# Optimization experiments

Measured on AMD Instinct MI355X. Metric: run time of the kernel, lower is better.

The kernel has to match this reference:

```python
import jax, jax.numpy as jnp
import numpy as np

LMAX = 4  # number of l blocks (lmax+1 in the original)
# segment ids mapping the L2 = sum(2l+1) = 16 spherical components to their l block
SEG = np.repeat(np.arange(LMAX), 2 * np.arange(LMAX) + 1)  # [16]
SEG_ONEHOT = np.eye(LMAX, dtype=np.float32)[SEG]  # [16, LMAX]


def setup_inputs() -> dict:
    key = jax.random.key(0)
    ks = jax.random.split(key, 10)
    b, m, f, k, L2 = 16, 64, 128, 64, 16
    def rnd(kk, shape, scale):
        return jax.random.normal(kk, shape, dtype=jnp.float32) * scale
    return {
        'x': rnd(ks[0], (b, m, f, L2), 1.0),
        'y': rnd(ks[1], (b, m, f, L2), 1.0),
        'wx0': rnd(ks[2], (k, f, f, LMAX), 1.0 / np.sqrt(f * f * LMAX)),
        'wy0': rnd(ks[3], (k, f, f, LMAX), 1.0 / np.sqrt(f * f * LMAX)),
        'wx_mlp': rnd(ks[4], (2, k, k), 1.0 / np.sqrt(k)),
        'bx_mlp': rnd(ks[5], (2, k, k), 0.02),
        'wy_mlp': rnd(ks[6], (2, k, k), 1.0 / np.sqrt(k)),
        'by_mlp': rnd(ks[7], (2, k, k), 0.02),
        'wxf': rnd(ks[8], (LMAX, f, k), 1.0 / np.sqrt(k)),
        'wyf': rnd(ks[9], (LMAX, f, k), 1.0 / np.sqrt(k)),
    }


def reference(x, y, wx0, wy0, wx_mlp, bx_mlp, wy_mlp, by_mlp, wxf, wyf):
    act = jax.nn.silu
    S = jnp.asarray(SEG_ONEHOT)  # [L2, lmax]
    # outer product of y and x features, segment-summed over each l block:
    # mix[b,m,fy,fx,l] = sum_c y[b,m,fy,c] * x[b,m,fx,c] * S[c,l]
    mix = jnp.einsum('bmfc,bmgc,cl->bmfgl', y, x, S)  # [b,m,f,f,lmax]
    mx = jnp.einsum('bmfgl,kfgl->bmk', mix, wx0)
    my = jnp.einsum('bmfgl,kfgl->bmk', mix, wy0)
    for i in range(wx_mlp.shape[0]):  # the n_mlp-1 used MLP stages
        mx = act(jnp.einsum('bmk,kl->bml', mx, wx_mlp[i]) + bx_mlp[i])
        my = act(jnp.einsum('bmk,kl->bml', my, wy_mlp[i]) + by_mlp[i])
    mx = act(jnp.einsum('bmk,lfk->bmfl', mx, wxf))  # [b,m,f,lmax]
    my = act(jnp.einsum('bmk,lfk->bmfl', my, wyf))
    # broadcast each l gate over its 2l+1 components (repeat == gather by SEG)
    seg = jnp.asarray(SEG)
    res = mx[..., seg] * x + my[..., seg] * y  # [b,m,f,L2]
    return res
```

## Files before the change

kernel.cpp:

```cpp
#include <hip/hip_runtime.h>
#include <stdint.h>


#define AS1 __attribute__((address_space(1)))
#define AS3 __attribute__((address_space(3)))

typedef __bf16 bf16x8 __attribute__((ext_vector_type(8)));
typedef float f32x4 __attribute__((ext_vector_type(4)));

__device__ __forceinline__ uint16_t f2b(float f) {
  uint32_t u = __float_as_uint(f);
  u += 0x7fffu + ((u >> 16) & 1u);
  return (uint16_t)(u >> 16);
}

#if __has_builtin(__builtin_amdgcn_fdot2_f32_bf16)
typedef __bf16 bf16x2 __attribute__((ext_vector_type(2)));
__device__ __forceinline__ float dot2b(uint32_t a, uint32_t b, float c) {
  union { uint32_t u; bf16x2 v; } ua, ub;
  ua.u = a; ub.u = b;
  return __builtin_amdgcn_fdot2_f32_bf16(ua.v, ub.v, c, false);
}
#else
__device__ __forceinline__ float dot2b(uint32_t a, uint32_t b, float c) {
  float a0 = __uint_as_float(a << 16), a1 = __uint_as_float(a & 0xffff0000u);
  float b0 = __uint_as_float(b << 16), b1 = __uint_as_float(b & 0xffff0000u);
  return c + a0 * b0 + a1 * b1;
}
#endif

__global__ __launch_bounds__(256) void convert_all(
    const float* __restrict__ wx0, const float* __restrict__ wy0,
    const float* __restrict__ x, const float* __restrict__ y,
    const float* __restrict__ wxf, const float* __restrict__ wyf,
    uint16_t* __restrict__ Wb2, uint16_t* __restrict__ xb,
    uint16_t* __restrict__ yb, float* __restrict__ wfT) {
  int bid = blockIdx.x, tid = threadIdx.x;
  if (bid < 4096) {
    int c = bid * 256 + tid;
    int fb = c >> 16;
    int rem = c & 65535;
    int fy = rem >> 9;
    int rem2 = rem & 511;
    int n = rem2 >> 2, pos = rem2 & 3;
    int slot = pos ^ ((n >> 1) & 3);
    int k = n & 63;
    const float* src = (n < 64 ? wx0 : wy0) +
        ((size_t)(k * 128 + fy) * 512 + fb * 32 + slot * 8);
    float4 v0 = *(const float4*)src;
    float4 v1 = *(const float4*)(src + 4);
    uint32_t o0 = (uint32_t)f2b(v0.x) | ((uint32_t)f2b(v0.y) << 16);
    uint32_t o1 = (uint32_t)f2b(v0.z) | ((uint32_t)f2b(v0.w) << 16);
    uint32_t o2 = (uint32_t)f2b(v1.x) | ((uint32_t)f2b(v1.y) << 16);
    uint32_t o3 = (uint32_t)f2b(v1.z) | ((uint32_t)f2b(v1.w) << 16);
    *(uint4*)(Wb2 + (size_t)c * 8) = make_uint4(o0, o1, o2, o3);
    return;
  }
  if (bid >= 6144) {
    int base = (bid - 6144) * 2048 + tid * 8;
#pragma unroll
    for (int ii = 0; ii < 8; ++ii) {
      int idx = base + ii;
      int side = idx >> 15, rem = idx & 32767;
      int k = rem >> 9, l = (rem >> 7) & 3, f = rem & 127;
      const float* src = side ? wyf : wxf;
      wfT[idx] = src[((size_t)l * 128 + f) * 64 + k];
    }
    return;
  }
  size_t i = ((size_t)(bid - 4096) * 256 + tid) * 8;
  const float* s; uint16_t* d;
  if (i < 2097152) { s = x + i;             d = xb + i; }
  else             { s = y + (i - 2097152); d = yb + (i - 2097152); }
  float4 v0 = *(const float4*)s;
  float4 v1 = *(const float4*)(s + 4);
  uint32_t o0 = (uint32_t)f2b(v0.x) | ((uint32_t)f2b(v0.y) << 16);
  uint32_t o1 = (uint32_t)f2b(v0.z) | ((uint32_t)f2b(v0.w) << 16);
  uint32_t o2 = (uint32_t)f2b(v1.x) | ((uint32_t)f2b(v1.y) << 16);
  uint32_t o3 = (uint32_t)f2b(v1.z) | ((uint32_t)f2b(v1.w) << 16);
  *(uint4*)d = make_uint4(o0, o1, o2, o3);
}

__device__ __forceinline__ void gload_lds16(const void* g, void* l) {
  __builtin_amdgcn_global_load_lds((const AS1 uint32_t*)g, (AS3 uint32_t*)l, 16, 0, 0);
}

#define PIPE_BAR(N) \
  asm volatile("s_waitcnt vmcnt(" #N ") lgkmcnt(0)\n\ts_barrier" ::: "memory")

__global__ __launch_bounds__(512, 4) void fused_gemm(
    const uint16_t* __restrict__ xb, const uint16_t* __restrict__ yb,
    const uint16_t* __restrict__ Wb2, float* __restrict__ Cpart) {
  __shared__ __align__(16) uint16_t sA[2][128 * 32];
  __shared__ __align__(16) uint16_t sB[3][128 * 32];
  __shared__ __align__(16) uint16_t yS[3][2048];

  int tid = threadIdx.x;
  int w = tid >> 6, lane = tid & 63;
  int g_id = blockIdx.x;
  int fb = g_id >> 2, fyg = g_id & 3;
  int FB = fb * 8;
  int fy0 = fyg * 32;
  int m0 = blockIdx.y * 128;
  int r = lane & 15, q = lane >> 4;
  int wm = w >> 2, wn = w & 3;
  int m_loc = tid & 127, quarter = tid >> 7;

  uint32_t xr[16];
  {
    const uint16_t* xp0 = xb + (size_t)(m0 + m_loc) * 2048 + (FB + quarter * 2) * 16;
#pragma unroll
    for (int j = 0; j < 4; ++j) {
      uint4 v = *(const uint4*)(xp0 + j * 8);
      xr[j * 4 + 0] = v.x; xr[j * 4 + 1] = v.y;
      xr[j * 4 + 2] = v.z; xr[j * 4 + 3] = v.w;
    }
  }

  f32x4 zero = {0.f, 0.f, 0.f, 0.f};
  f32x4 acc[4][2];
#pragma unroll
  for (int i = 0; i < 4; ++i)
#pragma unroll
    for (int j = 0; j < 2; ++j) acc[i][j] = zero;

  auto issueB = [&](uint16_t* dstB, int t) {
    if (w < 4) {
      size_t base = (size_t)(fb * 128 + fy0 + t) * 4096;
#pragma unroll
      for (int jj = 0; jj < 2; ++jj) {
        int blk = w * 2 + jj;
        gload_lds16(Wb2 + base + blk * 512 + lane * 8, dstB + blk * 512);
      }
    }
  };
  int ychunk = (w >> 1) & 1, ymbase = (w & 1) * 64;
  const uint16_t* ysrc_base = yb + (size_t)(m0 + ymbase + lane) * 2048 + ychunk * 8;
  int ydst_off = ychunk * 1024 + ymbase * 8;
  auto issueY = [&](uint16_t* dstY, int t) {
    if (w >= 4) gload_lds16(ysrc_base + (size_t)(fy0 + t) * 16, dstY + ydst_off);
  };

  auto computeG = [&](const uint16_t* srcY, float* gg) {
    uint4 ya = *(const uint4*)(srcY + m_loc * 8);
    uint4 yc = *(const uint4*)(srcY + 1024 + m_loc * 8);
    uint32_t yp[8] = {ya.x, ya.y, ya.z, ya.w, yc.x, yc.y, yc.z, yc.w};
    uint32_t yl0 = yp[0] & 0xffffu, yh0 = yp[0] & 0xffff0000u;
    uint32_t yl4 = yp[4] & 0xffffu, yh4 = yp[4] & 0xffff0000u;
#pragma unroll
    for (int fxp = 0; fxp < 2; ++fxp) {
      const uint32_t* xp = xr + fxp * 8;
      gg[fxp * 4 + 0] = dot2b(xp[0], yl0, 0.f);
      gg[fxp * 4 + 1] = dot2b(xp[1], yp[1], dot2b(xp[0], yh0, 0.f));
      gg[fxp * 4 + 2] = dot2b(xp[4], yl4,
                         dot2b(xp[3], yp[3], dot2b(xp[2], yp[2], 0.f)));
      gg[fxp * 4 + 3] = dot2b(xp[7], yp[7], dot2b(xp[6], yp[6],
                         dot2b(xp[5], yp[5], dot2b(xp[4], yh4, 0.f))));
    }
  };
  auto writeA = [&](uint16_t* dstA, const float* gg) {
    uint32_t o[4];
#pragma unroll
    for (int p = 0; p < 4; ++p)
      o[p] = (__float_as_uint(gg[2 * p]) >> 16) |
             (__float_as_uint(gg[2 * p + 1]) & 0xffff0000u);
    int pos = quarter ^ ((m_loc >> 1) & 3);
    *(uint4*)(dstA + m_loc * 32 + pos * 8) = make_uint4(o[0], o[1], o[2], o[3]);
  };

  float gg[8];
  issueY(yS[0], 0);
  __syncthreads();
  computeG(yS[0], gg);
  writeA(sA[0], gg);
  issueB(sB[0], 0);
  issueY(yS[1], 1);
  issueB(sB[1], 1);
  issueY(yS[2], 2);
  if (w < 4) PIPE_BAR(2); else PIPE_BAR(1);

  uint16_t *pAc = sA[0], *pAn = sA[1];
  uint16_t *pBread = sB[0], *pBmid = sB[1], *pBissue = sB[2];
  uint16_t *pYcomp = yS[1], *pYmid = yS[2], *pYissue = yS[0];

  for (int t = 0; t < 32; ++t) {
    if (t <= 29) issueB(pBissue, t + 2);
    if (t <= 28) issueY(pYissue, t + 3);

    bf16x8 a[4], b[2];
#pragma unroll
    for (int i = 0; i < 4; ++i) {
      int row = wm * 64 + i * 16 + r;
      int pos = q ^ ((row >> 1) & 3);
      a[i] = *(const bf16x8*)&pAc[row * 32 + pos * 8];
    }
#pragma unroll
    for (int j = 0; j < 2; ++j) {
      int row = wn * 32 + j * 16 + r;
      int pos = q ^ ((row >> 1) & 3);
      b[j] = *(const bf16x8*)&pBread[row * 32 + pos * 8];
    }

    if (t < 31) {
      computeG(pYcomp, gg);
      writeA(pAn, gg);
    }

    __builtin_amdgcn_s_setprio(1);
#pragma unroll
    for (int i = 0; i < 4; ++i)
#pragma unroll
      for (int j = 0; j < 2; ++j)
        acc[i][j] = __builtin_amdgcn_mfma_f32_16x16x32_bf16(a[i], b[j], acc[i][j], 0, 0, 0);
    __builtin_amdgcn_s_setprio(0);

    if (t <= 28)      { if (w < 4) PIPE_BAR(2); else PIPE_BAR(1); }
    else if (t == 29) { if (w < 4) PIPE_BAR(2); else PIPE_BAR(0); }
    else if (t == 30) PIPE_BAR(0);

    uint16_t* tp;
    tp = pAc; pAc = pAn; pAn = tp;
    tp = pBread; pBread = pBmid; pBmid = pBissue; pBissue = tp;
    tp = pYcomp; pYcomp = pYmid; pYmid = pYissue; pYissue = tp;
  }

  float* cbase = Cpart + (size_t)g_id * 131072;
#pragma unroll
  for (int i = 0; i < 4; ++i)
#pragma unroll
    for (int j = 0; j < 2; ++j)
#pragma unroll
      for (int reg = 0; reg < 4; ++reg) {
        int mm = m0 + wm * 64 + i * 16 + q * 4 + reg;
        int nn = wn * 32 + j * 16 + r;
        cbase[(size_t)mm * 128 + nn] = acc[i][j][reg];
      }
}

__global__ __launch_bounds__(256) void finish_kernel(
    const float* __restrict__ x, const float* __restrict__ y,
    const float* __restrict__ wx_mlp, const float* __restrict__ bx_mlp,
    const float* __restrict__ wy_mlp, const float* __restrict__ by_mlp,
    const float* __restrict__ wfT,
    const float* __restrict__ Cpart, float* __restrict__ out) {
  const int seg[16] = {0,1,1,1,2,2,2,2,2,3,3,3,3,3,3,3};
  __shared__ float sred[256];
  __shared__ float sm[128];
  __shared__ float sg[2][128][4];
  int t = threadIdx.x;
  int bm = blockIdx.x;
  int mi = bm & 63;

  {
    int col = t & 127, hh = t >> 7;
    const float* cp = Cpart + (size_t)(hh * 32) * 131072 + (size_t)bm * 128 + col;
    float s = 0.f;
#pragma unroll 8
    for (int sp = 0; sp < 32; ++sp)
      s += cp[(size_t)sp * 131072];
    sred[t] = s;
  }
  __syncthreads();
  if (t < 128) sm[t] = sred[t] + sred[t + 128];
  __syncthreads();

  for (int st = 0; st < 2; ++st) {
    float v = 0.f;
    if (t < 128) {
      int side = t >> 6, j = t & 63;
      const float* wmlp = side ? wy_mlp : wx_mlp;
      const float* bmlp = side ? by_mlp : bx_mlp;
      const float* mv = sm + side * 64;
#pragma unroll 8
      for (int k = 0; k < 64; ++k)
        v += mv[k] * wmlp[(st * 64 + k) * 64 + j];
      v += bmlp[(st * 64 + mi) * 64 + j];
      v = v / (1.f + __expf(-v));
    }
    __syncthreads();
    if (t < 128) sm[t] = v;
    __syncthreads();
  }

  {
    int side = t >> 7, f = t & 127;
    const float* base = wfT + side * 32768;
    const float* mv = sm + side * 64;
    float gg[4] = {0.f, 0.f, 0.f, 0.f};
#pragma unroll 8
    for (int k = 0; k < 64; ++k) {
      float m2 = mv[k];
#pragma unroll
      for (int l = 0; l < 4; ++l)
        gg[l] += m2 * base[(k * 4 + l) * 128 + f];
    }
#pragma unroll
    for (int l = 0; l < 4; ++l)
      sg[side][f][l] = gg[l] / (1.f + __expf(-gg[l]));
  }
  __syncthreads();

  {
    int f = t >> 1, half = t & 1;
    size_t base = ((size_t)bm * 128 + f) * 16 + half * 8;
    float4 xa = *(const float4*)(x + base), xb4 = *(const float4*)(x + base + 4);
    float4 ya = *(const float4*)(y + base), yb4 = *(const float4*)(y + base + 4);
    float xv[8] = {xa.x, xa.y, xa.z, xa.w, xb4.x, xb4.y, xb4.z, xb4.w};
    float yv[8] = {ya.x, ya.y, ya.z, ya.w, yb4.x, yb4.y, yb4.z, yb4.w};
    float o[8];
#pragma unroll
    for (int ii = 0; ii < 8; ++ii) {
      int c = half * 8 + ii;
      o[ii] = sg[0][f][seg[c]] * xv[ii] + sg[1][f][seg[c]] * yv[ii];
    }
    *(float4*)(out + base)     = make_float4(o[0], o[1], o[2], o[3]);
    *(float4*)(out + base + 4) = make_float4(o[4], o[5], o[6], o[7]);
  }
}

extern "C" void kernel_launch(void* const* d_in, const int* in_sizes, int n_in,
                              void* d_out, int out_size, void* d_ws, size_t ws_size,
                              hipStream_t stream) {
  const float* x      = (const float*)d_in[0];
  const float* y      = (const float*)d_in[1];
  const float* wx0    = (const float*)d_in[2];
  const float* wy0    = (const float*)d_in[3];
  const float* wx_mlp = (const float*)d_in[4];
  const float* bx_mlp = (const float*)d_in[5];
  const float* wy_mlp = (const float*)d_in[6];
  const float* by_mlp = (const float*)d_in[7];
  const float* wxf    = (const float*)d_in[8];
  const float* wyf    = (const float*)d_in[9];
  float* out = (float*)d_out;

  uint16_t* Wb2   = (uint16_t*)d_ws;
  uint16_t* xb    = (uint16_t*)((char*)d_ws + (size_t)16777216);
  uint16_t* yb    = (uint16_t*)((char*)d_ws + (size_t)20971520);
  float*    Cpart = (float*)((char*)d_ws + (size_t)25165824);
  float*    wfT   = (float*)((char*)d_ws + (size_t)58720256);

  convert_all<<<6176, 256, 0, stream>>>(wx0, wy0, x, y, wxf, wyf, Wb2, xb, yb, wfT);
  fused_gemm<<<dim3(64, 8), 512, 0, stream>>>(xb, yb, Wb2, Cpart);
  finish_kernel<<<1024, 256, 0, stream>>>(x, y, wx_mlp, bx_mlp, wy_mlp, by_mlp,
                                          wfT, Cpart, out);
}
```

Baseline: 166.1 us.

## Build GEMM A operand in registers, drop LDS staging, halve M tile

The fused GEMM now computes the segment-summed outer-product A fragments directly in each wave's registers, in the MFMA operand layout, and feeds them straight to MFMA. This removes the sA LDS buffer and its write/read round trip. Blocks shrink to 256 threads with 64-row M tiles, giving twice as many blocks, and the y and W loads are re-pipelined with two stages in flight. The weight conversion now reads the source contiguously and scatters its writes, so global reads are coalesced. In exchange each wave recomputes the A values it needs and holds more x data in registers.

```diff
diff --git a/kernel.cpp b/kernel.cpp
--- a/kernel.cpp
+++ b/kernel.cpp
@@ -37,23 +37,25 @@
     uint16_t* __restrict__ yb, float* __restrict__ wfT) {
   int bid = blockIdx.x, tid = threadIdx.x;
   if (bid < 4096) {
-    int c = bid * 256 + tid;
-    int fb = c >> 16;
-    int rem = c & 65535;
-    int fy = rem >> 9;
-    int rem2 = rem & 511;
-    int n = rem2 >> 2, pos = rem2 & 3;
-    int slot = pos ^ ((n >> 1) & 3);
-    int k = n & 63;
-    const float* src = (n < 64 ? wx0 : wy0) +
-        ((size_t)(k * 128 + fy) * 512 + fb * 32 + slot * 8);
+    size_t idx = ((size_t)bid * 256 + tid) * 8;
+    int side = idx >= 4194304 ? 1 : 0;
+    size_t rem = side ? idx - 4194304 : idx;
+    const float* src = (side ? wy0 : wx0) + rem;
     float4 v0 = *(const float4*)src;
     float4 v1 = *(const float4*)(src + 4);
+    int fx0 = (int)((rem >> 2) & 127);
+    int fy  = (int)((rem >> 9) & 127);
+    int k   = (int)(rem >> 16);
+    int n = side * 64 + k;
+    int fb = fx0 >> 3;
+    int slot = (fx0 >> 1) & 3;
+    int pos = slot ^ ((n >> 1) & 3);
     uint32_t o0 = (uint32_t)f2b(v0.x) | ((uint32_t)f2b(v0.y) << 16);
     uint32_t o1 = (uint32_t)f2b(v0.z) | ((uint32_t)f2b(v0.w) << 16);
     uint32_t o2 = (uint32_t)f2b(v1.x) | ((uint32_t)f2b(v1.y) << 16);
     uint32_t o3 = (uint32_t)f2b(v1.z) | ((uint32_t)f2b(v1.w) << 16);
-    *(uint4*)(Wb2 + (size_t)c * 8) = make_uint4(o0, o1, o2, o3);
+    size_t chunk = (((size_t)(fb * 128 + fy)) * 128 + n) * 4 + pos;
+    *(uint4*)(Wb2 + chunk * 8) = make_uint4(o0, o1, o2, o3);
     return;
   }
   if (bid >= 6144) {
@@ -88,12 +90,11 @@
 #define PIPE_BAR(N) \
   asm volatile("s_waitcnt vmcnt(" #N ") lgkmcnt(0)\n\ts_barrier" ::: "memory")
 
-__global__ __launch_bounds__(512, 4) void fused_gemm(
+__global__ __launch_bounds__(256, 4) void fused_gemm(
     const uint16_t* __restrict__ xb, const uint16_t* __restrict__ yb,
     const uint16_t* __restrict__ Wb2, float* __restrict__ Cpart) {
-  __shared__ __align__(16) uint16_t sA[2][128 * 32];
   __shared__ __align__(16) uint16_t sB[3][128 * 32];
-  __shared__ __align__(16) uint16_t yS[3][2048];
+  __shared__ __align__(16) uint16_t yS[3][1024];
 
   int tid = threadIdx.x;
   int w = tid >> 6, lane = tid & 63;
@@ -101,138 +102,114 @@
   int fb = g_id >> 2, fyg = g_id & 3;
   int FB = fb * 8;
   int fy0 = fyg * 32;
-  int m0 = blockIdx.y * 128;
+  int m0 = blockIdx.y * 64;
   int r = lane & 15, q = lane >> 4;
-  int wm = w >> 2, wn = w & 3;
-  int m_loc = tid & 127, quarter = tid >> 7;
-
-  uint32_t xr[16];
-  {
-    const uint16_t* xp0 = xb + (size_t)(m0 + m_loc) * 2048 + (FB + quarter * 2) * 16;
+  int wm = w >> 1, wn = w & 1;
+
+  uint32_t xreg[2][16];
+#pragma unroll
+  for (int i = 0; i < 2; ++i) {
+    const uint16_t* xp0 =
+        xb + (size_t)(m0 + wm * 32 + i * 16 + r) * 2048 + (FB + 2 * q) * 16;
+#pragma unroll
+    for (int j2 = 0; j2 < 4; ++j2) {
+      uint4 v = *(const uint4*)(xp0 + j2 * 8);
+      xreg[i][j2 * 4 + 0] = v.x; xreg[i][j2 * 4 + 1] = v.y;
+      xreg[i][j2 * 4 + 2] = v.z; xreg[i][j2 * 4 + 3] = v.w;
+    }
+  }
+
+  f32x4 zero = {0.f, 0.f, 0.f, 0.f};
+  f32x4 acc[2][4];
+#pragma unroll
+  for (int i = 0; i < 2; ++i)
+#pragma unroll
+    for (int j = 0; j < 4; ++j) acc[i][j] = zero;
+
+  int fbfy = fb * 128 + fy0;
+  auto issueB = [&](uint16_t* dstB, int t) {
+    size_t base = (size_t)(fbfy + t) * 4096;
+    gload_lds16(Wb2 + base + (size_t)(w * 2) * 512 + lane * 8,
+                dstB + (w * 2) * 512);
+    gload_lds16(Wb2 + base + (size_t)(w * 2 + 1) * 512 + lane * 8,
+                dstB + (w * 2 + 1) * 512);
+  };
+  const uint16_t* ysrc = yb + (size_t)(m0 + lane) * 2048 + w * 8;
+  auto issueY = [&](uint16_t* dstY, int t) {
+    if (w < 2) gload_lds16(ysrc + (size_t)(fy0 + t) * 16, dstY + w * 512);
+  };
+
+  issueB(sB[0], 0); issueY(yS[0], 0);
+  issueB(sB[1], 1); issueY(yS[1], 1);
+  if (w < 2) PIPE_BAR(3); else PIPE_BAR(2);
+
+  uint16_t *pB0 = sB[0], *pB1 = sB[1], *pB2 = sB[2];
+  uint16_t *pY0 = yS[0], *pY1 = yS[1], *pY2 = yS[2];
+
+  for (int t = 0; t < 32; ++t) {
+    if (t <= 29) { issueB(pB2, t + 2); issueY(pY2, t + 2); }
+
+    bf16x8 b[4];
 #pragma unroll
     for (int j = 0; j < 4; ++j) {
-      uint4 v = *(const uint4*)(xp0 + j * 8);
-      xr[j * 4 + 0] = v.x; xr[j * 4 + 1] = v.y;
-      xr[j * 4 + 2] = v.z; xr[j * 4 + 3] = v.w;
-    }
-  }
-
-  f32x4 zero = {0.f, 0.f, 0.f, 0.f};
-  f32x4 acc[4][2];
-#pragma unroll
-  for (int i = 0; i < 4; ++i)
-#pragma unroll
-    for (int j = 0; j < 2; ++j) acc[i][j] = zero;
-
-  auto issueB = [&](uint16_t* dstB, int t) {
-    if (w < 4) {
-      size_t base = (size_t)(fb * 128 + fy0 + t) * 4096;
-#pragma unroll
-      for (int jj = 0; jj < 2; ++jj) {
-        int blk = w * 2 + jj;
-        gload_lds16(Wb2 + base + blk * 512 + lane * 8, dstB + blk * 512);
+      int row = wn * 64 + j * 16 + r;
+      int pos = q ^ ((row >> 1) & 3);
+      b[j] = *(const bf16x8*)&pB0[row * 32 + pos * 8];
+    }
+    uint32_t yw[2][8];
+#pragma unroll
+    for (int i = 0; i < 2; ++i) {
+      int row = wm * 32 + i * 16 + r;
+      uint4 a0 = *(const uint4*)&pY0[row * 8];
+      uint4 a1 = *(const uint4*)&pY0[512 + row * 8];
+      yw[i][0] = a0.x; yw[i][1] = a0.y; yw[i][2] = a0.z; yw[i][3] = a0.w;
+      yw[i][4] = a1.x; yw[i][5] = a1.y; yw[i][6] = a1.z; yw[i][7] = a1.w;
+    }
+
+#pragma unroll
+    for (int i = 0; i < 2; ++i) {
+      uint32_t yl0 = yw[i][0] & 0xffffu, yh0 = yw[i][0] & 0xffff0000u;
+      uint32_t yl4 = yw[i][4] & 0xffffu, yh4 = yw[i][4] & 0xffff0000u;
+      union { uint32_t u[4]; bf16x8 v; } af;
+#pragma unroll
+      for (int fxp = 0; fxp < 2; ++fxp) {
+        const uint32_t* xp = &xreg[i][fxp * 8];
+        float g0 = dot2b(xp[0], yl0, 0.f);
+        float g1 = dot2b(xp[1], yw[i][1], dot2b(xp[0], yh0, 0.f));
+        float g2 = dot2b(xp[4], yl4,
+                    dot2b(xp[3], yw[i][3], dot2b(xp[2], yw[i][2], 0.f)));
+        float g3 = dot2b(xp[7], yw[i][7], dot2b(xp[6], yw[i][6],
+                    dot2b(xp[5], yw[i][5], dot2b(xp[4], yh4, 0.f))));
+        af.u[fxp * 2 + 0] = (__float_as_uint(g0) >> 16) |
+                            (__float_as_uint(g1) & 0xffff0000u);
+        af.u[fxp * 2 + 1] = (__float_as_uint(g2) >> 16) |
+                            (__float_as_uint(g3) & 0xffff0000u);
       }
-    }
-  };
-  int ychunk = (w >> 1) & 1, ymbase = (w & 1) * 64;
-  const uint16_t* ysrc_base = yb + (size_t)(m0 + ymbase + lane) * 2048 + ychunk * 8;
-  int ydst_off = ychunk * 1024 + ymbase * 8;
-  auto issueY = [&](uint16_t* dstY, int t) {
-    if (w >= 4) gload_lds16(ysrc_base + (size_t)(fy0 + t) * 16, dstY + ydst_off);
-  };
-
-  auto computeG = [&](const uint16_t* srcY, float* gg) {
-    uint4 ya = *(const uint4*)(srcY + m_loc * 8);
-    uint4 yc = *(const uint4*)(srcY + 1024 + m_loc * 8);
-    uint32_t yp[8] = {ya.x, ya.y, ya.z, ya.w, yc.x, yc.y, yc.z, yc.w};
-    uint32_t yl0 = yp[0] & 0xffffu, yh0 = yp[0] & 0xffff0000u;
-    uint32_t yl4 = yp[4] & 0xffffu, yh4 = yp[4] & 0xffff0000u;
-#pragma unroll
-    for (int fxp = 0; fxp < 2; ++fxp) {
-      const uint32_t* xp = xr + fxp * 8;
-      gg[fxp * 4 + 0] = dot2b(xp[0], yl0, 0.f);
-      gg[fxp * 4 + 1] = dot2b(xp[1], yp[1], dot2b(xp[0], yh0, 0.f));
-      gg[fxp * 4 + 2] = dot2b(xp[4], yl4,
-                         dot2b(xp[3], yp[3], dot2b(xp[2], yp[2], 0.f)));
-      gg[fxp * 4 + 3] = dot2b(xp[7], yp[7], dot2b(xp[6], yp[6],
-                         dot2b(xp[5], yp[5], dot2b(xp[4], yh4, 0.f))));
-    }
-  };
-  auto writeA = [&](uint16_t* dstA, const float* gg) {
-    uint32_t o[4];
-#pragma unroll
-    for (int p = 0; p < 4; ++p)
-      o[p] = (__float_as_uint(gg[2 * p]) >> 16) |
-             (__float_as_uint(gg[2 * p + 1]) & 0xffff0000u);
-    int pos = quarter ^ ((m_loc >> 1) & 3);
-    *(uint4*)(dstA + m_loc * 32 + pos * 8) = make_uint4(o[0], o[1], o[2], o[3]);
-  };
-
-  float gg[8];
-  issueY(yS[0], 0);
-  __syncthreads();
-  computeG(yS[0], gg);
-  writeA(sA[0], gg);
-  issueB(sB[0], 0);
-  issueY(yS[1], 1);
-  issueB(sB[1], 1);
-  issueY(yS[2], 2);
-  if (w < 4) PIPE_BAR(2); else PIPE_BAR(1);
-
-  uint16_t *pAc = sA[0], *pAn = sA[1];
-  uint16_t *pBread = sB[0], *pBmid = sB[1], *pBissue = sB[2];
-  uint16_t *pYcomp = yS[1], *pYmid = yS[2], *pYissue = yS[0];
-
-  for (int t = 0; t < 32; ++t) {
-    if (t <= 29) issueB(pBissue, t + 2);
-    if (t <= 28) issueY(pYissue, t + 3);
-
-    bf16x8 a[4], b[2];
-#pragma unroll
-    for (int i = 0; i < 4; ++i) {
-      int row = wm * 64 + i * 16 + r;
-      int pos = q ^ ((row >> 1) & 3);
-      a[i] = *(const bf16x8*)&pAc[row * 32 + pos * 8];
-    }
-#pragma unroll
-    for (int j = 0; j < 2; ++j) {
-      int row = wn * 32 + j * 16 + r;
-      int pos = q ^ ((row >> 1) & 3);
-      b[j] = *(const bf16x8*)&pBread[row * 32 + pos * 8];
-    }
-
-    if (t < 31) {
-      computeG(pYcomp, gg);
-      writeA(pAn, gg);
-    }
-
-    __builtin_amdgcn_s_setprio(1);
-#pragma unroll
-    for (int i = 0; i < 4; ++i)
-#pragma unroll
-      for (int j = 0; j < 2; ++j)
-        acc[i][j] = __builtin_amdgcn_mfma_f32_16x16x32_bf16(a[i], b[j], acc[i][j], 0, 0, 0);
-    __builtin_amdgcn_s_setprio(0);
-
-    if (t <= 28)      { if (w < 4) PIPE_BAR(2); else PIPE_BAR(1); }
-    else if (t == 29) { if (w < 4) PIPE_BAR(2); else PIPE_BAR(0); }
+      __builtin_amdgcn_s_setprio(1);
+#pragma unroll
+      for (int j = 0; j < 4; ++j)
+        acc[i][j] = __builtin_amdgcn_mfma_f32_16x16x32_bf16(af.v, b[j],
+                                                            acc[i][j], 0, 0, 0);
+      __builtin_amdgcn_s_setprio(0);
+    }
+
+    if (t <= 29)      { if (w < 2) PIPE_BAR(3); else PIPE_BAR(2); }
     else if (t == 30) PIPE_BAR(0);
 
     uint16_t* tp;
-    tp = pAc; pAc = pAn; pAn = tp;
-    tp = pBread; pBread = pBmid; pBmid = pBissue; pBissue = tp;
-    tp = pYcomp; pYcomp = pYmid; pYmid = pYissue; pYissue = tp;
+    tp = pB0; pB0 = pB1; pB1 = pB2; pB2 = tp;
+    tp = pY0; pY0 = pY1; pY1 = pY2; pY2 = tp;
   }
 
   float* cbase = Cpart + (size_t)g_id * 131072;
 #pragma unroll
-  for (int i = 0; i < 4; ++i)
-#pragma unroll
-    for (int j = 0; j < 2; ++j)
+  for (int i = 0; i < 2; ++i)
+#pragma unroll
+    for (int j = 0; j < 4; ++j)
 #pragma unroll
       for (int reg = 0; reg < 4; ++reg) {
-        int mm = m0 + wm * 64 + i * 16 + q * 4 + reg;
-        int nn = wn * 32 + j * 16 + r;
+        int mm = m0 + wm * 32 + i * 16 + q * 4 + reg;
+        int nn = wn * 64 + j * 16 + r;
         cbase[(size_t)mm * 128 + nn] = acc[i][j][reg];
       }
 }
@@ -340,7 +317,7 @@
   float*    wfT   = (float*)((char*)d_ws + (size_t)58720256);
 
   convert_all<<<6176, 256, 0, stream>>>(wx0, wy0, x, y, wxf, wyf, Wb2, xb, yb, wfT);
-  fused_gemm<<<dim3(64, 8), 512, 0, stream>>>(xb, yb, Wb2, Cpart);
+  fused_gemm<<<dim3(64, 16), 256, 0, stream>>>(xb, yb, Wb2, Cpart);
   finish_kernel<<<1024, 256, 0, stream>>>(x, y, wx_mlp, bx_mlp, wy_mlp, by_mlp,
                                           wfT, Cpart, out);
 }
```

New measurement: 171.9 us. 1.04x slower.

## Shrink LDS pipeline to double buffering and raise occupancy hint

Applied to the files above, without the earlier changes.

Cuts the B and Y shared-memory staging from triple to double buffering and replaces the hand-written waitcnt/barrier with plain __syncthreads. The launch bound rises to 8 blocks per CU, and the B-tile loads are spread across all eight waves, one load each, instead of four waves doing two. The aim is to fit more resident blocks and hide latency through occupancy rather than pipeline depth. The cost is a shallower prefetch distance and stronger barriers that wait for all outstanding memory operations every iteration.

```diff
diff --git a/kernel.cpp b/kernel.cpp
--- a/kernel.cpp
+++ b/kernel.cpp
@@ -85,15 +85,12 @@
   __builtin_amdgcn_global_load_lds((const AS1 uint32_t*)g, (AS3 uint32_t*)l, 16, 0, 0);
 }
 
-#define PIPE_BAR(N) \
-  asm volatile("s_waitcnt vmcnt(" #N ") lgkmcnt(0)\n\ts_barrier" ::: "memory")
-
-__global__ __launch_bounds__(512, 4) void fused_gemm(
+__global__ __launch_bounds__(512, 8) void fused_gemm(
     const uint16_t* __restrict__ xb, const uint16_t* __restrict__ yb,
     const uint16_t* __restrict__ Wb2, float* __restrict__ Cpart) {
   __shared__ __align__(16) uint16_t sA[2][128 * 32];
-  __shared__ __align__(16) uint16_t sB[3][128 * 32];
-  __shared__ __align__(16) uint16_t yS[3][2048];
+  __shared__ __align__(16) uint16_t sB[2][128 * 32];
+  __shared__ __align__(16) uint16_t yS[2][2048];
 
   int tid = threadIdx.x;
   int w = tid >> 6, lane = tid & 63;
@@ -125,20 +122,14 @@
     for (int j = 0; j < 2; ++j) acc[i][j] = zero;
 
   auto issueB = [&](uint16_t* dstB, int t) {
-    if (w < 4) {
-      size_t base = (size_t)(fb * 128 + fy0 + t) * 4096;
-#pragma unroll
-      for (int jj = 0; jj < 2; ++jj) {
-        int blk = w * 2 + jj;
-        gload_lds16(Wb2 + base + blk * 512 + lane * 8, dstB + blk * 512);
-      }
-    }
+    size_t base = (size_t)(fb * 128 + fy0 + t) * 4096;
+    gload_lds16(Wb2 + base + (size_t)w * 512 + lane * 8, dstB + w * 512);
   };
   int ychunk = (w >> 1) & 1, ymbase = (w & 1) * 64;
   const uint16_t* ysrc_base = yb + (size_t)(m0 + ymbase + lane) * 2048 + ychunk * 8;
   int ydst_off = ychunk * 1024 + ymbase * 8;
   auto issueY = [&](uint16_t* dstY, int t) {
-    if (w >= 4) gload_lds16(ysrc_base + (size_t)(fy0 + t) * 16, dstY + ydst_off);
+    if (w < 4) gload_lds16(ysrc_base + (size_t)(fy0 + t) * 16, dstY + ydst_off);
   };
 
   auto computeG = [&](const uint16_t* srcY, float* gg) {
@@ -170,22 +161,18 @@
 
   float gg[8];
   issueY(yS[0], 0);
+  issueY(yS[1], 1);
+  issueB(sB[0], 0);
   __syncthreads();
   computeG(yS[0], gg);
   writeA(sA[0], gg);
-  issueB(sB[0], 0);
-  issueY(yS[1], 1);
-  issueB(sB[1], 1);
-  issueY(yS[2], 2);
-  if (w < 4) PIPE_BAR(2); else PIPE_BAR(1);
-
-  uint16_t *pAc = sA[0], *pAn = sA[1];
-  uint16_t *pBread = sB[0], *pBmid = sB[1], *pBissue = sB[2];
-  uint16_t *pYcomp = yS[1], *pYmid = yS[2], *pYissue = yS[0];
+  __syncthreads();
 
   for (int t = 0; t < 32; ++t) {
-    if (t <= 29) issueB(pBissue, t + 2);
-    if (t <= 28) issueY(pYissue, t + 3);
+    uint16_t* pAc = sA[t & 1];
+    uint16_t* pBc = sB[t & 1];
+    if (t < 31) issueB(sB[(t + 1) & 1], t + 1);
+    if (t < 30) issueY(yS[t & 1], t + 2);
 
     bf16x8 a[4], b[2];
 #pragma unroll
@@ -198,12 +185,12 @@
     for (int j = 0; j < 2; ++j) {
       int row = wn * 32 + j * 16 + r;
       int pos = q ^ ((row >> 1) & 3);
-      b[j] = *(const bf16x8*)&pBread[row * 32 + pos * 8];
+      b[j] = *(const bf16x8*)&pBc[row * 32 + pos * 8];
     }
 
     if (t < 31) {
-      computeG(pYcomp, gg);
-      writeA(pAn, gg);
+      computeG(yS[(t + 1) & 1], gg);
+      writeA(sA[(t + 1) & 1], gg);
     }
 
     __builtin_amdgcn_s_setprio(1);
@@ -214,14 +201,7 @@
         acc[i][j] = __builtin_amdgcn_mfma_f32_16x16x32_bf16(a[i], b[j], acc[i][j], 0, 0, 0);
     __builtin_amdgcn_s_setprio(0);
 
-    if (t <= 28)      { if (w < 4) PIPE_BAR(2); else PIPE_BAR(1); }
-    else if (t == 29) { if (w < 4) PIPE_BAR(2); else PIPE_BAR(0); }
-    else if (t == 30) PIPE_BAR(0);
-
-    uint16_t* tp;
-    tp = pAc; pAc = pAn; pAn = tp;
-    tp = pBread; pBread = pBmid; pBmid = pBissue; pBissue = tp;
-    tp = pYcomp; pYcomp = pYmid; pYmid = pYissue; pYissue = tp;
+    if (t < 31) __syncthreads();
   }
 
   float* cbase = Cpart + (size_t)g_id * 131072;
```

New measurement: 377.9 us. 128% more time.
